# Kernel tuning notes

Measured on AMD Instinct MI355X. Metric: run time of the kernel, lower is better.

Reference implementation:

```python
import jax, jax.numpy as jnp
import numpy as np

WS = 8  # window_size


def _gridify(x, ws):
    # [B,C,H,W] -> [B,C,Hc,Wc,ws*ws], matching torch unfold(2,ws,ws).unfold(3,ws,ws)
    B, C, H, W = x.shape
    Hc, Wc = H // ws, W // ws
    return (x.reshape(B, C, Hc, ws, Wc, ws)
             .transpose(0, 1, 2, 4, 3, 5)
             .reshape(B, C, Hc, Wc, ws * ws))


def setup_inputs() -> dict:
    key = jax.random.key(0)
    x = jax.random.normal(key, (8, 1, 2048, 2048), dtype=jnp.float32)
    return {"x": x}


def reference(x):
    ws = WS
    B, C, H, W = x.shape
    Hc, Wc = H // ws, W // ws

    grid = _gridify(x, ws)  # [B,1,Hc,Wc,ws^2] logits per window

    k_cat, k_bern = jax.random.split(jax.random.key(42))

    # Categorical sample via Gumbel-max over window logits
    g = jax.random.gumbel(k_cat, grid.shape, grid.dtype)
    choices = jnp.argmax(grid + g, axis=-1)  # [B,1,Hc,Wc] int

    logsm = jax.nn.log_softmax(grid, axis=-1)
    cat_lp = jnp.take_along_axis(logsm, choices[..., None], axis=-1)[..., 0]
    selected = jnp.take_along_axis(grid, choices[..., None], axis=-1)[..., 0]

    # Bernoulli acceptance with logits = selected
    u = jax.random.uniform(k_bern, selected.shape, selected.dtype)
    accepted = (u < jax.nn.sigmoid(selected)).astype(grid.dtype)
    bern_lp = (accepted * jax.nn.log_sigmoid(selected)
               + (1.0 - accepted) * jax.nn.log_sigmoid(-selected))

    log_probs = (cat_lp + bern_lp)[:, 0]       # [B,Hc,Wc]
    mask = accepted[:, 0] > 0                   # [B,Hc,Wc] bool

    # Keypoint coords: window cell origin + in-window offset (row-major flatten)
    ch = choices[:, 0]                          # [B,Hc,Wc]
    di = ch // ws
    dj = ch % ws
    rows = jnp.arange(Hc, dtype=ch.dtype)[None, :, None] * ws + di
    cols = jnp.arange(Wc, dtype=ch.dtype)[None, None, :] * ws + dj
    # torch returns keypoints[...,(row,col)].flip(-1) -> (col,row) i.e. (x,y)
    kp_xy = jnp.stack([cols, rows], axis=-1).astype(jnp.float32)  # [B,Hc,Wc,2]

    # Dense equivalent of the ragged per-batch output: valid entries are where
    # mask is True (the torch version compacts kp_xy[b][mask[b]], log_probs[b][mask[b]]).
    return kp_xy, log_probs, mask
```

## Files before the change

kernel.cpp:

```cpp
#include <hip/hip_runtime.h>
#include <stdint.h>
#include <math.h>

#define TFR(r) { x0 += x1; x1 = (x1 << r) | (x1 >> (32 - r)); x1 ^= x0; }

__host__ __device__ __forceinline__ void tf20(uint32_t ks0, uint32_t ks1, uint32_t ks2,
                                              uint32_t x0, uint32_t x1,
                                              uint32_t& o0, uint32_t& o1) {
  x0 += ks0; x1 += ks1;
  TFR(13) TFR(15) TFR(26) TFR(6)
  x0 += ks1; x1 += ks2 + 1u;
  TFR(17) TFR(29) TFR(16) TFR(24)
  x0 += ks2; x1 += ks0 + 2u;
  TFR(13) TFR(15) TFR(26) TFR(6)
  x0 += ks0; x1 += ks1 + 3u;
  TFR(17) TFR(29) TFR(16) TFR(24)
  x0 += ks1; x1 += ks2 + 4u;
  TFR(13) TFR(15) TFR(26) TFR(6)
  x0 += ks2; x1 += ks0 + 5u;
  o0 = x0; o1 = x1;
}

__device__ __forceinline__ uint32_t tf20_fold(uint32_t ks0, uint32_t ks1, uint32_t ks2,
                                              uint32_t x0, uint32_t x1) {
  TFR(13) TFR(15) TFR(26) TFR(6)
  x0 += ks1; x1 += ks2 + 1u;
  TFR(17) TFR(29) TFR(16) TFR(24)
  x0 += ks2; x1 += ks0 + 2u;
  TFR(13) TFR(15) TFR(26) TFR(6)
  x0 += ks0; x1 += ks1 + 3u;
  TFR(17) TFR(29) TFR(16) TFR(24)
  x0 += ks1; x1 += ks2 + 4u;
  TFR(13) TFR(15) TFR(26) TFR(6)
  x0 += ks2; x1 += ks0 + 5u;
  return x0 ^ x1;
}

__device__ __forceinline__ float bits_to_u01(uint32_t bits) {
  return __uint_as_float((bits >> 9) | 0x3f800000u) - 1.0f;
}

__device__ __forceinline__ float ex2(float z) {
#if defined(__has_builtin)
#if __has_builtin(__builtin_amdgcn_exp2f)
  return __builtin_amdgcn_exp2f(z);
#else
  return exp2f(z);
#endif
#else
  return exp2f(z);
#endif
}

__global__ __launch_bounds__(256) void kp_kernel(
    const float* __restrict__ x, float* __restrict__ out,
    uint32_t kc0, uint32_t kc1, uint32_t kb0, uint32_t kb1) {
  const int wc = threadIdx.x;
  const int bh = blockIdx.x;
  const int b  = bh >> 8;
  const int hc = bh & 255;

  const float* base = x + ((size_t)(b * 2048) + (size_t)(hc * 8)) * 2048 + (size_t)(wc * 8);

  const uint32_t kc2 = kc0 ^ kc1 ^ 0x1BD11BDAu;
  const uint32_t kb2 = kb0 ^ kb1 ^ 0x1BD11BDAu;
  const uint32_t w   = ((uint32_t)bh << 8) | (uint32_t)wc;
  const uint32_t jb  = w << 6;
  const uint32_t jk1 = jb + kc1;

  const float L2E = 1.4426950408889634f;

  float m  = -INFINITY;
  float s2 = 0.0f;
  float best = -INFINITY;
  uint32_t bk = 0u;

  for (int di = 0; di < 8; ++di) {
    const float4* p = reinterpret_cast<const float4*>(base + (size_t)di * 2048);
    float4 a = p[0];
    float4 c = p[1];
    float vv[8] = {a.x, a.y, a.z, a.w, c.x, c.y, c.z, c.w};

    float gm = vv[0];
#pragma unroll
    for (int j = 1; j < 8; ++j) gm = fmaxf(gm, vv[j]);
    float gmL = gm * L2E;
    float gs = 0.0f;
#pragma unroll
    for (int j = 0; j < 8; ++j) gs += ex2(fmaf(vv[j], L2E, -gmL));
    float mn = fmaxf(m, gm);
    s2 = s2 * ex2((m - mn) * L2E) + gs * ex2((gm - mn) * L2E);
    m = mn;

#pragma unroll
    for (int j = 0; j < 8; ++j) {
      uint32_t bits = tf20_fold(kc0, kc1, kc2, kc0, jk1 + (uint32_t)(di * 8 + j));
      float u = bits_to_u01(bits);
      u = fmaxf(u, 1.17549435e-38f);
      float wv = logf(-logf(u));
      float pv = vv[j] - wv;
      if (pv > best) { best = pv; bk = (uint32_t)(di * 8 + j); }
    }
  }

  const float sel = base[(size_t)(bk >> 3) * 2048 + (bk & 7u)];

  uint32_t b0, b1;
  tf20(kb0, kb1, kb2, 0u, w, b0, b1);
  float ub = bits_to_u01(b0 ^ b1);
  double sd = (double)sel;
  double ed = exp(-sd);
  float sigf = (float)(1.0 / (1.0 + ed));
  bool acc = ub < sigf;

  float l1 = log1pf((float)ed);
  float bern_lp = acc ? -l1 : -(sel + l1);

  float cat_lp = (sel - m) - logf(s2);
  float lp = cat_lp + bern_lp;

  float col = (float)((wc << 3) | (int)(bk & 7u));
  float row = (float)((hc << 3) | (int)(bk >> 3));

  reinterpret_cast<float2*>(out)[w] = make_float2(col, row);
  out[1048576u + w] = lp;
  out[1572864u + w] = acc ? 1.0f : 0.0f;
}

extern "C" void kernel_launch(void* const* d_in, const int* in_sizes, int n_in,
                              void* d_out, int out_size, void* d_ws, size_t ws_size,
                              hipStream_t stream) {
  const float* x = (const float*)d_in[0];
  float* out = (float*)d_out;

  const uint32_t k0 = 0u, k1 = 42u;
  const uint32_t k2 = k0 ^ k1 ^ 0x1BD11BDAu;
  uint32_t kc0, kc1, kb0, kb1;
  tf20(k0, k1, k2, 0u, 0u, kc0, kc1);
  tf20(k0, k1, k2, 0u, 1u, kb0, kb1);

  kp_kernel<<<2048, 256, 0, stream>>>(x, out, kc0, kc1, kb0, kb1);
}
```

Before: 249.5 us.

## Use fast hardware log2 for Gumbel noise with exact fallback on near-ties

Replaces the two accurate logf calls per element in the Gumbel transform with hardware log2 intrinsics scaled by ln2. Tracks the runner-up score and reruns the exact logf path when the top two are within a small margin, so the argmax should match the reference. The online softmax rescaling is replaced by a two-pass max then sum-of-exp that re-reads the window, using two accumulators. This trades extra global re-reads and a divergent fallback branch for cheaper transcendentals in the hot loop.

```diff
diff --git a/kernel.cpp b/kernel.cpp
--- a/kernel.cpp
+++ b/kernel.cpp
@@ -41,14 +41,17 @@
 }
 
 __device__ __forceinline__ float ex2(float z) {
-#if defined(__has_builtin)
 #if __has_builtin(__builtin_amdgcn_exp2f)
   return __builtin_amdgcn_exp2f(z);
 #else
   return exp2f(z);
 #endif
+}
+__device__ __forceinline__ float lg2(float z) {
+#if __has_builtin(__builtin_amdgcn_logf)
+  return __builtin_amdgcn_logf(z);
 #else
-  return exp2f(z);
+  return __log2f(z);
 #endif
 }
 
@@ -65,14 +68,14 @@
   const uint32_t kc2 = kc0 ^ kc1 ^ 0x1BD11BDAu;
   const uint32_t kb2 = kb0 ^ kb1 ^ 0x1BD11BDAu;
   const uint32_t w   = ((uint32_t)bh << 8) | (uint32_t)wc;
-  const uint32_t jb  = w << 6;
-  const uint32_t jk1 = jb + kc1;
+  const uint32_t jk1 = (w << 6) + kc1;
 
-  const float L2E = 1.4426950408889634f;
+  const float L2E  = 1.4426950408889634f;
+  const float LN2  = 0.69314718f;
+  const float TINY = 1.17549435e-38f;
 
-  float m  = -INFINITY;
-  float s2 = 0.0f;
-  float best = -INFINITY;
+  float m = -INFINITY;
+  float best = -INFINITY, sec = -INFINITY;
   uint32_t bk = 0u;
 
   for (int di = 0; di < 8; ++di) {
@@ -81,27 +84,59 @@
     float4 c = p[1];
     float vv[8] = {a.x, a.y, a.z, a.w, c.x, c.y, c.z, c.w};
 
-    float gm = vv[0];
 #pragma unroll
-    for (int j = 1; j < 8; ++j) gm = fmaxf(gm, vv[j]);
-    float gmL = gm * L2E;
-    float gs = 0.0f;
-#pragma unroll
-    for (int j = 0; j < 8; ++j) gs += ex2(fmaf(vv[j], L2E, -gmL));
-    float mn = fmaxf(m, gm);
-    s2 = s2 * ex2((m - mn) * L2E) + gs * ex2((gm - mn) * L2E);
-    m = mn;
+    for (int j = 0; j < 8; ++j) m = fmaxf(m, vv[j]);
 
 #pragma unroll
     for (int j = 0; j < 8; ++j) {
       uint32_t bits = tf20_fold(kc0, kc1, kc2, kc0, jk1 + (uint32_t)(di * 8 + j));
-      float u = bits_to_u01(bits);
-      u = fmaxf(u, 1.17549435e-38f);
-      float wv = logf(-logf(u));
+      float u  = fmaxf(bits_to_u01(bits), TINY);
+      float t  = lg2(u) * (-LN2);
+      float wv = lg2(t) * LN2;
       float pv = vv[j] - wv;
-      if (pv > best) { best = pv; bk = (uint32_t)(di * 8 + j); }
+      bool gt = pv > best;
+      sec  = gt ? best : fmaxf(sec, pv);
+      best = gt ? pv : best;
+      bk   = gt ? (uint32_t)(di * 8 + j) : bk;
     }
   }
+
+  if (best - sec <= 1e-4f) {
+    float bb = -INFINITY;
+    uint32_t bkx = 0u;
+    for (int di = 0; di < 8; ++di) {
+      const float4* p = reinterpret_cast<const float4*>(base + (size_t)di * 2048);
+      float4 a = p[0];
+      float4 c = p[1];
+      float vv[8] = {a.x, a.y, a.z, a.w, c.x, c.y, c.z, c.w};
+#pragma unroll
+      for (int j = 0; j < 8; ++j) {
+        uint32_t bits = tf20_fold(kc0, kc1, kc2, kc0, jk1 + (uint32_t)(di * 8 + j));
+        float u  = fmaxf(bits_to_u01(bits), TINY);
+        float wv = logf(-logf(u));
+        float pv = vv[j] - wv;
+        if (pv > bb) { bb = pv; bkx = (uint32_t)(di * 8 + j); }
+      }
+    }
+    bk = bkx;
+  }
+
+  const float mL = m * L2E;
+  float s2a = 0.0f, s2b = 0.0f;
+  for (int di = 0; di < 8; ++di) {
+    const float4* p = reinterpret_cast<const float4*>(base + (size_t)di * 2048);
+    float4 a = p[0];
+    float4 c = p[1];
+    s2a += ex2(fmaf(a.x, L2E, -mL));
+    s2b += ex2(fmaf(a.y, L2E, -mL));
+    s2a += ex2(fmaf(a.z, L2E, -mL));
+    s2b += ex2(fmaf(a.w, L2E, -mL));
+    s2a += ex2(fmaf(c.x, L2E, -mL));
+    s2b += ex2(fmaf(c.y, L2E, -mL));
+    s2a += ex2(fmaf(c.z, L2E, -mL));
+    s2b += ex2(fmaf(c.w, L2E, -mL));
+  }
+  const float s2 = s2a + s2b;
 
   const float sel = base[(size_t)(bk >> 3) * 2048 + (bk & 7u)];
 
```

Result: no change. 246.7 us (-1.1%).
